# Kernel tuning notes

Hardware: AMD Instinct MI355X
Metric: run time of the kernel (lower is better)

Reference implementation:

```python
import jax, jax.numpy as jnp
import numpy as np

EPS = 1e-7
C_IN = 1.0
C_ATTN = 1.0
C_OUT = 1.0
B, N, D_IN, H, D_OUT = 4, 2048, 128, 8, 64  # in_features = D_IN+1, ambient A = D_OUT+1
INIT_BOUND = 0.02


def _lift(spatial, c):
    # lift spatial coords to hyperboloid of curvature c: x0 = sqrt(1/c + ||x_s||^2)
    time = jnp.sqrt(1.0 / c + jnp.sum(spatial * spatial, axis=-1, keepdims=True))
    return jnp.concatenate([time, spatial], axis=-1)


def _lorentz_normalize(mu, c):
    # project weighted sum back onto hyperboloid: mu / (sqrt(c) * sqrt(|<mu,mu>_L|))
    lor = -mu[..., 0:1] ** 2 + jnp.sum(mu[..., 1:] ** 2, axis=-1, keepdims=True)
    return mu / (jnp.sqrt(c) * jnp.sqrt(jnp.clip(-lor, EPS)))


def setup_inputs() -> dict:
    key = jax.random.key(0)
    ks = jax.random.split(key, 8)
    x_spatial = jax.random.normal(ks[0], (B, N, D_IN), dtype=jnp.float32) * 0.5
    x = _lift(x_spatial, C_IN)  # valid hyperboloid points, curvature C_IN
    u = lambda k, shp: jax.random.uniform(k, shp, minval=-INIT_BOUND, maxval=INIT_BOUND, dtype=jnp.float32)
    return {
        "x": x,
        "Wq": u(ks[1], (H, D_IN + 1, D_OUT)),
        "Wk": u(ks[2], (H, D_IN + 1, D_OUT)),
        "Wv": u(ks[3], (H, D_IN + 1, D_OUT)),
        "bq": u(ks[4], (H, D_OUT)),
        "bk": u(ks[5], (H, D_OUT)),
        "bv": u(ks[6], (H, D_OUT)),
        "scale": jnp.array(1.0, dtype=jnp.float32),
        "attn_bias": jnp.array(0.0, dtype=jnp.float32),
    }


def reference(x, Wq, Wk, Wv, bq, bk, bv, scale, attn_bias):
    # HTCLinear per head (vectorized over heads): spatial = x @ W + b, lift to curvature C_ATTN
    def proj(W, b):
        s = jnp.einsum('bni,hid->bnhd', x, W) + b  # (B,N,H,D_OUT)
        return _lift(s, C_ATTN)                    # (B,N,H,D_OUT+1)

    q = proj(Wq, bq)
    k = proj(Wk, bk)
    v = proj(Wv, bv)

    # Lorentzian inner product scores: -q0*k0 + q_s . k_s  -> (B,N,H,M)
    li = (-jnp.einsum('bnh,bmh->bnhm', q[..., 0], k[..., 0])
          + jnp.einsum('bnhd,bmhd->bnhm', q[..., 1:], k[..., 1:]))
    scores = (2.0 + 2.0 * li) / (scale + EPS) + attn_bias
    w = jax.nn.softmax(scores, axis=-1)

    # Lorentz midpoint aggregation over keys
    mu = jnp.einsum('bnhm,bmha->bnha', w, v)
    mid = _lorentz_normalize(mu, C_ATTN)  # (B,N,H,A)

    # uniform Lorentz midpoint over heads (weights 1/H)
    avg = jnp.mean(mid, axis=2)           # (B,N,A)
    out = _lorentz_normalize(avg, C_ATTN)

    # spatial_to_hyperboloid: rescale curvature C_ATTN -> C_OUT and re-lift
    spatial = out[..., 1:] * jnp.sqrt(C_ATTN / C_OUT)
    return _lift(spatial, C_OUT)  # (B,N,D_OUT+1)
```

## Files before the change

kernel.cpp:

```cpp
#include <hip/hip_runtime.h>
#include <hip/hip_bf16.h>

typedef __bf16 bf16x8 __attribute__((ext_vector_type(8)));
typedef float f32x16 __attribute__((ext_vector_type(16)));
typedef unsigned int u32;
typedef unsigned short u16;
typedef u32 u32x2 __attribute__((ext_vector_type(2)));
typedef u32 u32x4 __attribute__((ext_vector_type(4)));

static constexpr int Nn  = 2048;
static constexpr int DIN = 129;
static constexpr int QP  = 80;
static constexpr int AMB = 65;
static constexpr int XP  = 144;
static constexpr int NS  = 2;
static constexpr int PR  = 72;
static constexpr int KROW = 88;
static constexpr int KTS  = 3072;
static constexpr int VROW = 40;
static constexpr int VTS  = 4096;
static constexpr float LOG2E = 1.4426950408889634f;

#define DEV static __device__ __forceinline__

#if __has_builtin(__builtin_amdgcn_exp2f)
#define FEXP2 __builtin_amdgcn_exp2f
#else
#define FEXP2 exp2f
#endif

DEV u16 f2bf(float f) {
  union { __bf16 h; u16 u; } c;
  c.h = (__bf16)f;
  return c.u;
}
DEV float bf2f(u16 u) {
  union { float f; u32 uu; } c;
  c.uu = ((u32)u) << 16;
  return c.f;
}
DEV u32 cvtpk(float a, float b) {
  u32 r;
  asm("v_cvt_pk_bf16_f32 %0, %1, %2" : "=v"(r) : "v"(a), "v"(b));
  return r;
}
DEV void swap32(u32& a, u32& b) {
  asm("v_permlane32_swap_b32 %0, %1" : "+v"(a), "+v"(b));
}
DEV void gload_lds16(const u16* g, u16* l) {
  __builtin_amdgcn_global_load_lds(
      (const __attribute__((address_space(1))) unsigned int*)g,
      (__attribute__((address_space(3))) unsigned int*)l, 16, 0, 0);
}

__global__ __launch_bounds__(256) void prep_k(const float* __restrict__ x,
                                              u16* __restrict__ xb) {
  const int t = blockIdx.x * 256 + threadIdx.x;
  const int row = t / 18, cg = t % 18;
  u16 tmp[8];
#pragma unroll
  for (int j = 0; j < 8; ++j) {
    const int c = cg * 8 + j;
    tmp[j] = (c < DIN) ? f2bf(x[(size_t)row * DIN + c])
                       : (c == DIN ? f2bf(1.0f) : (u16)0);
  }
  u32x4 w;
  w[0] = (u32)tmp[0] | ((u32)tmp[1] << 16);
  w[1] = (u32)tmp[2] | ((u32)tmp[3] << 16);
  w[2] = (u32)tmp[4] | ((u32)tmp[5] << 16);
  w[3] = (u32)tmp[6] | ((u32)tmp[7] << 16);
  *((u32x4*)xb + t) = w;
}

__global__ __launch_bounds__(256) void proj_k(
    const u16* __restrict__ xb,
    const float* __restrict__ Wq, const float* __restrict__ Wk, const float* __restrict__ Wv,
    const float* __restrict__ bq, const float* __restrict__ bk, const float* __restrict__ bv,
    const float* __restrict__ scale_p,
    u16* __restrict__ Qb, u16* __restrict__ Ktl, u16* __restrict__ Vtl) {
  __shared__ u16 wt[64][152];
  __shared__ __align__(16) u16 tiles[4][2816];

  const int tid = threadIdx.x;
  const int wid = tid >> 6, l = tid & 63;
  const int z = blockIdx.y;
  const int T = z >> 3, h = z & 7;
  const float* W    = (T == 0 ? Wq : (T == 1 ? Wk : Wv)) + (size_t)h * DIN * 64;
  const float* bias = (T == 0 ? bq : (T == 1 ? bk : bv)) + h * 64;

  {
    const int d = tid & 63, kk = tid >> 6;
    for (int k = kk; k < XP; k += 4)
      wt[d][k] = (k < DIN) ? f2bf(W[(size_t)k * 64 + d])
                           : (k == DIN ? f2bf(bias[d]) : (u16)0);
  }
  __syncthreads();

  const int lo = l & 31, hi = l >> 5;
  const float alpha = 2.0f * LOG2E / (scale_p[0] + 1e-7f);
  u16* tl = &tiles[wid][0];

#pragma unroll 1
  for (int rt = 0; rt < 2; ++rt) {
    const int row0 = (blockIdx.x * 8 + wid * 2 + rt) * 32;
    const u16* xr = xb + (size_t)(row0 + lo) * XP;

    f32x16 acc0 = {}, acc1 = {};
#pragma unroll
    for (int s = 0; s < 9; ++s) {
      bf16x8 a  = *(const bf16x8*)&xr[16 * s + 8 * hi];
      bf16x8 b0 = *(const bf16x8*)&wt[lo][16 * s + 8 * hi];
      bf16x8 b1 = *(const bf16x8*)&wt[32 + lo][16 * s + 8 * hi];
      acc0 = __builtin_amdgcn_mfma_f32_32x32x16_bf16(b0, a, acc0, 0, 0, 0);
      acc1 = __builtin_amdgcn_mfma_f32_32x32x16_bf16(b1, a, acc1, 0, 0, 0);
    }

    float nrm = 0.f;
#pragma unroll
    for (int r = 0; r < 16; ++r) nrm += acc0[r] * acc0[r] + acc1[r] * acc1[r];
    nrm += __shfl_xor(nrm, 32);
    const float time = sqrtf(1.0f + nrm);

    if (T == 0) {
#pragma unroll
      for (int g = 0; g < 4; ++g) {
        const u32 w0 = cvtpk(alpha * acc0[4 * g],     alpha * acc0[4 * g + 1]);
        const u32 w1 = cvtpk(alpha * acc0[4 * g + 2], alpha * acc0[4 * g + 3]);
        const u32 w2 = cvtpk(alpha * acc1[4 * g],     alpha * acc1[4 * g + 1]);
        const u32 w3 = cvtpk(alpha * acc1[4 * g + 2], alpha * acc1[4 * g + 3]);
        *(u32x2*)&tl[lo * 80 + 8 * g + 4 * hi]      = (u32x2){w0, w1};
        *(u32x2*)&tl[lo * 80 + 32 + 8 * g + 4 * hi] = (u32x2){w2, w3};
      }
      if (hi == 0) *(u32x4*)&tl[lo * 80 + 64] = (u32x4){(u32)f2bf(alpha * time), 0, 0, 0};
      else         *(u32x4*)&tl[lo * 80 + 72] = (u32x4){0, 0, 0, 0};
    } else if (T == 1) {
#pragma unroll
      for (int g = 0; g < 4; ++g) {
        const u32 w0 = cvtpk(acc0[4 * g],     acc0[4 * g + 1]);
        const u32 w1 = cvtpk(acc0[4 * g + 2], acc0[4 * g + 3]);
        const u32 w2 = cvtpk(acc1[4 * g],     acc1[4 * g + 1]);
        const u32 w3 = cvtpk(acc1[4 * g + 2], acc1[4 * g + 3]);
        *(u32x2*)&tl[lo * 88 + 8 * g + 4 * hi]      = (u32x2){w0, w1};
        *(u32x2*)&tl[lo * 88 + 32 + 8 * g + 4 * hi] = (u32x2){w2, w3};
      }
      if (hi == 0) *(u32x4*)&tl[lo * 88 + 64] = (u32x4){(u32)f2bf(-(time - 1.0f)), 0, 0, 0};
      else         *(u32x4*)&tl[lo * 88 + 72] = (u32x4){0, 0, 0, 0};
    } else {
#pragma unroll
      for (int r = 0; r < 16; ++r) {
        const int d = (r & 3) + 8 * (r >> 2) + 4 * hi;
        tl[d * 40 + lo]        = f2bf(acc0[r]);
        tl[(32 + d) * 40 + lo] = f2bf(acc1[r]);
      }
      if (hi == 0) tl[64 * 40 + lo] = f2bf(time);
    }

    const int b = row0 >> 11, n0 = row0 & 2047;
    const int bh = b * 8 + h;
    u16* gdst;
    int nch;
    if (T == 0) { gdst = Qb + ((size_t)bh * Nn + n0) * QP;                nch = 320; }
    else if (T == 1) { gdst = Ktl + (size_t)bh * 64 * KTS + (size_t)(n0 >> 5) * KTS; nch = 352; }
    else { gdst = Vtl + (size_t)bh * 64 * VTS + (size_t)(n0 >> 5) * VTS;  nch = 325; }
    for (int j = l; j < nch; j += 64)
      *(u32x4*)(gdst + j * 8) = *(const u32x4*)(tl + j * 8);
  }
}

DEV void stage_super(const u16* kg, const u16* vg, u16* kl, u16* vl,
                     const int w, const int lane) {
  if (w == 0) {
#pragma unroll
    for (int i = 0; i < 6; ++i) gload_lds16(kg + i * 512 + lane * 8, kl + i * 512);
    gload_lds16(vg + lane * 8, vl);
  } else if (w == 1) {
#pragma unroll
    for (int i = 1; i < 8; ++i) gload_lds16(vg + i * 512 + lane * 8, vl + i * 512);
  } else if (w == 2) {
#pragma unroll
    for (int i = 6; i < 12; ++i) gload_lds16(kg + i * 512 + lane * 8, kl + i * 512);
    gload_lds16(vg + 8 * 512 + lane * 8, vl + 8 * 512);
  } else {
#pragma unroll
    for (int i = 9; i < 16; ++i) gload_lds16(vg + i * 512 + lane * 8, vl + i * 512);
  }
}

DEV void waitbar() {
  asm volatile("s_waitcnt vmcnt(0) lgkmcnt(0)\ns_barrier" ::: "memory");
}

DEV void exp_pack(const f32x16 sc, bf16x8& fA, bf16x8& fB) {
  float p[16];
#pragma unroll
  for (int r = 0; r < 16; ++r) p[r] = FEXP2(sc[r]);
  u32 a0 = cvtpk(p[0], p[1]),  a1 = cvtpk(p[2], p[3]);
  u32 a2 = cvtpk(p[4], p[5]),  a3 = cvtpk(p[6], p[7]);
  u32 c0 = cvtpk(p[8], p[9]),  c1 = cvtpk(p[10], p[11]);
  u32 c2 = cvtpk(p[12], p[13]), c3 = cvtpk(p[14], p[15]);
  swap32(a0, a2);
  swap32(a1, a3);
  swap32(c0, c2);
  swap32(c1, c3);
  union { u32x4 u; bf16x8 b; } ca, cb;
  ca.u = (u32x4){a0, a1, a2, a3};
  cb.u = (u32x4){c0, c1, c2, c3};
  fA = ca.b;
  fB = cb.b;
}

DEV void compute_tile64(const u16* kl, const u16* vl, const int lo, const int hi,
                        const bf16x8 (&qA)[5], const bf16x8 (&qB)[5],
                        f32x16& a0, f32x16& a1, f32x16& a2,
                        f32x16& b0, f32x16& b1, f32x16& b2) {
  f32x16 sA = {}, sB = {};
  __builtin_amdgcn_s_setprio(1);
#pragma unroll
  for (int s = 0; s < 5; ++s) {
    const bf16x8 kf = *(const bf16x8*)&kl[lo * KROW + 16 * s + 8 * hi];
    sA = __builtin_amdgcn_mfma_f32_32x32x16_bf16(kf, qA[s], sA, 0, 0, 0);
    sB = __builtin_amdgcn_mfma_f32_32x32x16_bf16(kf, qB[s], sB, 0, 0, 0);
  }
  __builtin_amdgcn_s_setprio(0);
  bf16x8 fA0, fB0, fA1, fB1;
  exp_pack(sA, fA0, fB0);
  exp_pack(sB, fA1, fB1);
  __builtin_amdgcn_s_setprio(1);
#pragma unroll
  for (int t = 0; t < 3; ++t) {
    const bf16x8 va = *(const bf16x8*)&vl[(32 * t + lo) * VROW + 8 * hi];
    const bf16x8 vb = *(const bf16x8*)&vl[(32 * t + lo) * VROW + 16 + 8 * hi];
    f32x16& oa = (t == 0 ? a0 : (t == 1 ? a1 : a2));
    f32x16& ob = (t == 0 ? b0 : (t == 1 ? b1 : b2));
    oa = __builtin_amdgcn_mfma_f32_32x32x16_bf16(va, fA0, oa, 0, 0, 0);
    oa = __builtin_amdgcn_mfma_f32_32x32x16_bf16(vb, fB0, oa, 0, 0, 0);
    ob = __builtin_amdgcn_mfma_f32_32x32x16_bf16(va, fA1, ob, 0, 0, 0);
    ob = __builtin_amdgcn_mfma_f32_32x32x16_bf16(vb, fB1, ob, 0, 0, 0);
  }
  __builtin_amdgcn_s_setprio(0);
}

DEV void write_partial(u16* part, const int bh, const int sidx, const int q,
                       const int hi, const f32x16& o0, const f32x16& o1,
                       const f32x16& o2) {
  u16* po = part + ((size_t)((bh * NS + sidx) * Nn + q)) * PR;
#pragma unroll
  for (int t = 0; t < 4; ++t) {
    const u32 a0 = cvtpk(o0[4 * t], o0[4 * t + 1]);
    const u32 a1 = cvtpk(o0[4 * t + 2], o0[4 * t + 3]);
    const u32 b0 = cvtpk(o1[4 * t], o1[4 * t + 1]);
    const u32 b1 = cvtpk(o1[4 * t + 2], o1[4 * t + 3]);
    *(u32x2*)&po[8 * t + 4 * hi]      = (u32x2){a0, a1};
    *(u32x2*)&po[8 * t + 4 * hi + 32] = (u32x2){b0, b1};
  }
  if (hi == 0) po[64] = f2bf(o2[0]);
}

__global__ __launch_bounds__(256, 2) void attn_k(
    const u16* __restrict__ Qb, const u16* __restrict__ Ktl,
    const u16* __restrict__ Vtl, u16* __restrict__ part) {
  __shared__ u16 kls[2][2 * KTS];
  __shared__ u16 vls[2][2 * VTS];

  const int tid  = threadIdx.x;
  const int w    = tid >> 6, lane = tid & 63;
  const int lo   = lane & 31, hi = lane >> 5;

  const u32 bid = blockIdx.x;
  const u32 swz = (bid & 7) * 64 + (bid >> 3);
  const int bh   = swz >> 4;
  const int sidx = (swz >> 3) & 1;
  const int qt   = swz & 7;
  const int qbase = qt * 256 + w * 64;

  const u16* qrowA = Qb + ((size_t)bh * Nn + qbase + lo) * QP;
  const u16* qrowB = qrowA + 32 * QP;
  bf16x8 qA[5], qB[5];
#pragma unroll
  for (int s = 0; s < 5; ++s) {
    qA[s] = *(const bf16x8*)&qrowA[16 * s + 8 * hi];
    qB[s] = *(const bf16x8*)&qrowB[16 * s + 8 * hi];
  }

  f32x16 a0 = {}, a1 = {}, a2 = {};
  f32x16 b0 = {}, b1 = {}, b2 = {};
  const u16* ktb = Ktl + (size_t)bh * 64 * KTS + (size_t)(sidx * 32) * KTS;
  const u16* vtb = Vtl + (size_t)bh * 64 * VTS + (size_t)(sidx * 32) * VTS;

  stage_super(ktb, vtb, kls[0], vls[0], w, lane);
  waitbar();

#pragma unroll 1
  for (int s = 0; s < 16; ++s) {
    const int pf = (s + 1 < 16) ? s + 1 : 15;
    stage_super(ktb + (size_t)pf * 2 * KTS, vtb + (size_t)pf * 2 * VTS,
                kls[(s + 1) & 1], vls[(s + 1) & 1], w, lane);
    compute_tile64(kls[s & 1],       vls[s & 1],       lo, hi, qA, qB, a0, a1, a2, b0, b1, b2);
    compute_tile64(kls[s & 1] + KTS, vls[s & 1] + VTS, lo, hi, qA, qB, a0, a1, a2, b0, b1, b2);
    waitbar();
  }

  write_partial(part, bh, sidx, qbase + lo,      hi, a0, a1, a2);
  write_partial(part, bh, sidx, qbase + 32 + lo, hi, b0, b1, b2);
}

__global__ __launch_bounds__(256) void finale_k(const u16* __restrict__ part,
                                                float* __restrict__ out) {
  const int tid = threadIdx.x;
  const int wv = tid >> 6, l = tid & 63;
  const int g = blockIdx.x * 4 + wv;
  const int b = g >> 11, n = g & 2047;
  const int h = l >> 3, c = l & 7;

  const u16* rowp = part + ((size_t)((b * 8 + h) * NS) * Nn + n) * PR;
  float Oh[8];
#pragma unroll
  for (int j = 0; j < 8; ++j) Oh[j] = 0.f;
  float th = 0.f;
#pragma unroll
  for (int s = 0; s < NS; ++s) {
    const u16* rp = rowp + (size_t)s * Nn * PR;
    const u32x4 v = *(const u32x4*)&rp[8 * c];
#pragma unroll
    for (int i = 0; i < 4; ++i) {
      union { u32 u; float f; } a, bb;
      a.u  = v[i] << 16;
      bb.u = v[i] & 0xffff0000u;
      Oh[2 * i]     += a.f;
      Oh[2 * i + 1] += bb.f;
    }
    th += bf2f(rp[64]);
  }

  float sq = 0.f;
#pragma unroll
  for (int j = 0; j < 8; ++j) sq += Oh[j] * Oh[j];
  sq += __shfl_xor(sq, 1);
  sq += __shfl_xor(sq, 2);
  sq += __shfl_xor(sq, 4);
  const float invh = rsqrtf(fmaxf(th * th - sq, 1e-7f));

  float S[8];
#pragma unroll
  for (int j = 0; j < 8; ++j) S[j] = Oh[j] * invh;
  float T = th * invh;
#pragma unroll
  for (int m = 8; m <= 32; m <<= 1) {
#pragma unroll
    for (int j = 0; j < 8; ++j) S[j] += __shfl_xor(S[j], m);
    T += __shfl_xor(T, m);
  }

  float s2 = 0.f;
#pragma unroll
  for (int j = 0; j < 8; ++j) s2 += S[j] * S[j];
  s2 += __shfl_xor(s2, 1);
  s2 += __shfl_xor(s2, 2);
  s2 += __shfl_xor(s2, 4);
  const float inv = rsqrtf(fmaxf(T * T - s2, 1e-7f));
  const float ssp = s2 * inv * inv;

  float* o = out + (size_t)g * AMB;
  if (h == 0) {
#pragma unroll
    for (int j = 0; j < 8; ++j) o[1 + 8 * c + j] = S[j] * inv;
    if (l == 0) o[0] = sqrtf(1.0f + ssp);
  }
}

extern "C" void kernel_launch(void* const* d_in, const int* in_sizes, int n_in,
                              void* d_out, int out_size, void* d_ws, size_t ws_size,
                              hipStream_t stream) {
  (void)in_sizes; (void)n_in; (void)out_size; (void)ws_size;
  const float* x  = (const float*)d_in[0];
  const float* Wq = (const float*)d_in[1];
  const float* Wk = (const float*)d_in[2];
  const float* Wv = (const float*)d_in[3];
  const float* bq = (const float*)d_in[4];
  const float* bk = (const float*)d_in[5];
  const float* bv = (const float*)d_in[6];
  const float* sc = (const float*)d_in[7];

  char* ws = (char*)d_ws;
  u16*  Qb  = (u16*)(ws);
  u16*  Ktl = (u16*)(ws + 10485760);
  u16*  Vtl = (u16*)(ws + 23068672);
  u16*  pb  = (u16*)(ws + 39845888);
  u16*  xb  = (u16*)(ws + 39845888);
  float* out = (float*)d_out;

  hipLaunchKernelGGL(prep_k, dim3(576), dim3(256), 0, stream, x, xb);
  hipLaunchKernelGGL(proj_k, dim3(32, 24), dim3(256), 0, stream,
                     xb, Wq, Wk, Wv, bq, bk, bv, sc, Qb, Ktl, Vtl);
  hipLaunchKernelGGL(attn_k, dim3(512), dim3(256), 0, stream, Qb, Ktl, Vtl, pb);
  hipLaunchKernelGGL(finale_k, dim3(2048), dim3(256), 0, stream, pb, out);
}
```

Measured before the change: 84.36 us.

## Split attention keys into four chunks with single-tile staging and higher occupancy

Raises the key-split factor from 2 to 4, so the attention grid doubles to 1024 blocks. Each block now handles 16 single 64-key tiles instead of 16 double-tile steps. LDS buffers shrink to one tile per stage and launch bounds request 4 blocks per CU. The aim is better CU occupancy and more latency hiding on a 256-CU device. In exchange, partial-output traffic doubles and the finale kernel must merge more partials.

After: 265.3 us. +214.5%, slower.

```diff
diff --git a/kernel.cpp b/kernel.cpp
--- a/kernel.cpp
+++ b/kernel.cpp
@@ -13,7 +13,7 @@
 static constexpr int QP  = 80;
 static constexpr int AMB = 65;
 static constexpr int XP  = 144;
-static constexpr int NS  = 2;
+static constexpr int NS  = 4;
 static constexpr int PR  = 72;
 static constexpr int KROW = 88;
 static constexpr int KTS  = 3072;
@@ -167,22 +167,19 @@
   }
 }
 
-DEV void stage_super(const u16* kg, const u16* vg, u16* kl, u16* vl,
-                     const int w, const int lane) {
-  if (w == 0) {
-#pragma unroll
-    for (int i = 0; i < 6; ++i) gload_lds16(kg + i * 512 + lane * 8, kl + i * 512);
-    gload_lds16(vg + lane * 8, vl);
-  } else if (w == 1) {
-#pragma unroll
-    for (int i = 1; i < 8; ++i) gload_lds16(vg + i * 512 + lane * 8, vl + i * 512);
-  } else if (w == 2) {
-#pragma unroll
-    for (int i = 6; i < 12; ++i) gload_lds16(kg + i * 512 + lane * 8, kl + i * 512);
-    gload_lds16(vg + 8 * 512 + lane * 8, vl + 8 * 512);
+DEV void stage_tile(const u16* kg, const u16* vg, u16* kl, u16* vl,
+                    const int w, const int lane) {
+  if (w < 2) {
+#pragma unroll
+    for (int i = 0; i < 3; ++i)
+      gload_lds16(kg + (w * 3 + i) * 512 + lane * 8, kl + (w * 3 + i) * 512);
+    gload_lds16(vg + w * 512 + lane * 8, vl + w * 512);
   } else {
 #pragma unroll
-    for (int i = 9; i < 16; ++i) gload_lds16(vg + i * 512 + lane * 8, vl + i * 512);
+    for (int i = 0; i < 3; ++i) {
+      const int j = (w - 2) * 3 + 2 + i;
+      gload_lds16(vg + j * 512 + lane * 8, vl + j * 512);
+    }
   }
 }
 
@@ -256,20 +253,20 @@
   if (hi == 0) po[64] = f2bf(o2[0]);
 }
 
-__global__ __launch_bounds__(256, 2) void attn_k(
+__global__ __launch_bounds__(256, 4) void attn_k(
     const u16* __restrict__ Qb, const u16* __restrict__ Ktl,
     const u16* __restrict__ Vtl, u16* __restrict__ part) {
-  __shared__ u16 kls[2][2 * KTS];
-  __shared__ u16 vls[2][2 * VTS];
+  __shared__ u16 kls[2][KTS];
+  __shared__ u16 vls[2][VTS];
 
   const int tid  = threadIdx.x;
   const int w    = tid >> 6, lane = tid & 63;
   const int lo   = lane & 31, hi = lane >> 5;
 
   const u32 bid = blockIdx.x;
-  const u32 swz = (bid & 7) * 64 + (bid >> 3);
-  const int bh   = swz >> 4;
-  const int sidx = (swz >> 3) & 1;
+  const u32 swz = (bid & 7) * 128 + (bid >> 3);
+  const int bh   = swz >> 5;
+  const int sidx = (swz >> 3) & 3;
   const int qt   = swz & 7;
   const int qbase = qt * 256 + w * 64;
 
@@ -284,19 +281,18 @@
 
   f32x16 a0 = {}, a1 = {}, a2 = {};
   f32x16 b0 = {}, b1 = {}, b2 = {};
-  const u16* ktb = Ktl + (size_t)bh * 64 * KTS + (size_t)(sidx * 32) * KTS;
-  const u16* vtb = Vtl + (size_t)bh * 64 * VTS + (size_t)(sidx * 32) * VTS;
-
-  stage_super(ktb, vtb, kls[0], vls[0], w, lane);
+  const u16* ktb = Ktl + (size_t)bh * 64 * KTS + (size_t)(sidx * 16) * KTS;
+  const u16* vtb = Vtl + (size_t)bh * 64 * VTS + (size_t)(sidx * 16) * VTS;
+
+  stage_tile(ktb, vtb, kls[0], vls[0], w, lane);
   waitbar();
 
 #pragma unroll 1
-  for (int s = 0; s < 16; ++s) {
-    const int pf = (s + 1 < 16) ? s + 1 : 15;
-    stage_super(ktb + (size_t)pf * 2 * KTS, vtb + (size_t)pf * 2 * VTS,
-                kls[(s + 1) & 1], vls[(s + 1) & 1], w, lane);
-    compute_tile64(kls[s & 1],       vls[s & 1],       lo, hi, qA, qB, a0, a1, a2, b0, b1, b2);
-    compute_tile64(kls[s & 1] + KTS, vls[s & 1] + VTS, lo, hi, qA, qB, a0, a1, a2, b0, b1, b2);
+  for (int t = 0; t < 16; ++t) {
+    const int pf = (t + 1 < 16) ? t + 1 : 15;
+    stage_tile(ktb + (size_t)pf * KTS, vtb + (size_t)pf * VTS,
+               kls[(t + 1) & 1], vls[(t + 1) & 1], w, lane);
+    compute_tile64(kls[t & 1], vls[t & 1], lo, hi, qA, qB, a0, a1, a2, b0, b1, b2);
     waitbar();
   }
 
@@ -392,6 +388,6 @@
   hipLaunchKernelGGL(prep_k, dim3(576), dim3(256), 0, stream, x, xb);
   hipLaunchKernelGGL(proj_k, dim3(32, 24), dim3(256), 0, stream,
                      xb, Wq, Wk, Wv, bq, bk, bv, sc, Qb, Ktl, Vtl);
-  hipLaunchKernelGGL(attn_k, dim3(512), dim3(256), 0, stream, Qb, Ktl, Vtl, pb);
+  hipLaunchKernelGGL(attn_k, dim3(1024), dim3(256), 0, stream, Qb, Ktl, Vtl, pb);
   hipLaunchKernelGGL(finale_k, dim3(2048), dim3(256), 0, stream, pb, out);
 }
```

## Compute time-coordinate row with VALU dot instead of a third MFMA tile

Applied to the files above, without the earlier changes.

The third PV MFMA tile, which existed only to produce the single time-coordinate row of V, is removed. That row is now accumulated with scalar FMAs from the fp32 exp values, followed by a cross-half shuffle reduction. V staging shrinks to 6 chunks per tile and is redistributed evenly across the four waves, reducing LDS footprint and global traffic. This saves a third of the PV MFMAs but adds VALU work and LDS reads in the softmax section.

New measurement: 84.57 us. About the same (+0.2%).

```diff
diff --git a/kernel.cpp b/kernel.cpp
--- a/kernel.cpp
+++ b/kernel.cpp
@@ -19,6 +19,7 @@
 static constexpr int KTS  = 3072;
 static constexpr int VROW = 40;
 static constexpr int VTS  = 4096;
+static constexpr int VLT  = 3072;
 static constexpr float LOG2E = 1.4426950408889634f;
 
 #define DEV static __device__ __forceinline__
@@ -37,6 +38,16 @@
 DEV float bf2f(u16 u) {
   union { float f; u32 uu; } c;
   c.uu = ((u32)u) << 16;
+  return c.f;
+}
+DEV float lo16f(u32 u) {
+  union { float f; u32 uu; } c;
+  c.uu = u << 16;
+  return c.f;
+}
+DEV float hi16f(u32 u) {
+  union { float f; u32 uu; } c;
+  c.uu = u & 0xffff0000u;
   return c.f;
 }
 DEV u32 cvtpk(float a, float b) {
@@ -172,17 +183,15 @@
   if (w == 0) {
 #pragma unroll
     for (int i = 0; i < 6; ++i) gload_lds16(kg + i * 512 + lane * 8, kl + i * 512);
-    gload_lds16(vg + lane * 8, vl);
   } else if (w == 1) {
 #pragma unroll
-    for (int i = 1; i < 8; ++i) gload_lds16(vg + i * 512 + lane * 8, vl + i * 512);
+    for (int i = 0; i < 6; ++i) gload_lds16(kg + KTS + i * 512 + lane * 8, kl + KTS + i * 512);
   } else if (w == 2) {
 #pragma unroll
-    for (int i = 6; i < 12; ++i) gload_lds16(kg + i * 512 + lane * 8, kl + i * 512);
-    gload_lds16(vg + 8 * 512 + lane * 8, vl + 8 * 512);
+    for (int i = 0; i < 6; ++i) gload_lds16(vg + i * 512 + lane * 8, vl + i * 512);
   } else {
 #pragma unroll
-    for (int i = 9; i < 16; ++i) gload_lds16(vg + i * 512 + lane * 8, vl + i * 512);
+    for (int i = 0; i < 6; ++i) gload_lds16(vg + VTS + i * 512 + lane * 8, vl + VLT + i * 512);
   }
 }
 
@@ -190,29 +199,10 @@
   asm volatile("s_waitcnt vmcnt(0) lgkmcnt(0)\ns_barrier" ::: "memory");
 }
 
-DEV void exp_pack(const f32x16 sc, bf16x8& fA, bf16x8& fB) {
-  float p[16];
-#pragma unroll
-  for (int r = 0; r < 16; ++r) p[r] = FEXP2(sc[r]);
-  u32 a0 = cvtpk(p[0], p[1]),  a1 = cvtpk(p[2], p[3]);
-  u32 a2 = cvtpk(p[4], p[5]),  a3 = cvtpk(p[6], p[7]);
-  u32 c0 = cvtpk(p[8], p[9]),  c1 = cvtpk(p[10], p[11]);
-  u32 c2 = cvtpk(p[12], p[13]), c3 = cvtpk(p[14], p[15]);
-  swap32(a0, a2);
-  swap32(a1, a3);
-  swap32(c0, c2);
-  swap32(c1, c3);
-  union { u32x4 u; bf16x8 b; } ca, cb;
-  ca.u = (u32x4){a0, a1, a2, a3};
-  cb.u = (u32x4){c0, c1, c2, c3};
-  fA = ca.b;
-  fB = cb.b;
-}
-
 DEV void compute_tile64(const u16* kl, const u16* vl, const int lo, const int hi,
                         const bf16x8 (&qA)[5], const bf16x8 (&qB)[5],
-                        f32x16& a0, f32x16& a1, f32x16& a2,
-                        f32x16& b0, f32x16& b1, f32x16& b2) {
+                        f32x16& a0, f32x16& a1, f32x16& b0, f32x16& b1,
+                        float& ta, float& tb) {
   f32x16 sA = {}, sB = {};
   __builtin_amdgcn_s_setprio(1);
 #pragma unroll
@@ -222,16 +212,48 @@
     sB = __builtin_amdgcn_mfma_f32_32x32x16_bf16(kf, qB[s], sB, 0, 0, 0);
   }
   __builtin_amdgcn_s_setprio(0);
-  bf16x8 fA0, fB0, fA1, fB1;
-  exp_pack(sA, fA0, fB0);
-  exp_pack(sB, fA1, fB1);
+
+  float pa[16], pb[16];
+#pragma unroll
+  for (int r = 0; r < 16; ++r) pa[r] = FEXP2(sA[r]);
+#pragma unroll
+  for (int r = 0; r < 16; ++r) pb[r] = FEXP2(sB[r]);
+
+  const u16* v0p = vl + 2560 + 4 * hi;
+#pragma unroll
+  for (int g = 0; g < 4; ++g) {
+    const u32x2 vv = *(const u32x2*)&v0p[8 * g];
+    const float v0 = lo16f(vv[0]), v1 = hi16f(vv[0]);
+    const float v2 = lo16f(vv[1]), v3 = hi16f(vv[1]);
+    ta += pa[4 * g] * v0 + pa[4 * g + 1] * v1 + pa[4 * g + 2] * v2 + pa[4 * g + 3] * v3;
+    tb += pb[4 * g] * v0 + pb[4 * g + 1] * v1 + pb[4 * g + 2] * v2 + pb[4 * g + 3] * v3;
+  }
+
+  u32 x0 = cvtpk(pa[0], pa[1]),   x1 = cvtpk(pa[2], pa[3]);
+  u32 x2 = cvtpk(pa[4], pa[5]),   x3 = cvtpk(pa[6], pa[7]);
+  u32 y0 = cvtpk(pa[8], pa[9]),   y1 = cvtpk(pa[10], pa[11]);
+  u32 y2 = cvtpk(pa[12], pa[13]), y3 = cvtpk(pa[14], pa[15]);
+  swap32(x0, x2); swap32(x1, x3); swap32(y0, y2); swap32(y1, y3);
+  union { u32x4 u; bf16x8 b; } cA0, cB0, cA1, cB1;
+  cA0.u = (u32x4){x0, x1, x2, x3};
+  cB0.u = (u32x4){y0, y1, y2, y3};
+  u32 z0 = cvtpk(pb[0], pb[1]),   z1 = cvtpk(pb[2], pb[3]);
+  u32 z2 = cvtpk(pb[4], pb[5]),   z3 = cvtpk(pb[6], pb[7]);
+  u32 t0 = cvtpk(pb[8], pb[9]),   t1 = cvtpk(pb[10], pb[11]);
+  u32 t2 = cvtpk(pb[12], pb[13]), t3 = cvtpk(pb[14], pb[15]);
+  swap32(z0, z2); swap32(z1, z3); swap32(t0, t2); swap32(t1, t3);
+  cA1.u = (u32x4){z0, z1, z2, z3};
+  cB1.u = (u32x4){t0, t1, t2, t3};
+  const bf16x8 fA0 = cA0.b, fB0 = cB0.b;
+  const bf16x8 fA1 = cA1.b, fB1 = cB1.b;
+
   __builtin_amdgcn_s_setprio(1);
 #pragma unroll
-  for (int t = 0; t < 3; ++t) {
+  for (int t = 0; t < 2; ++t) {
     const bf16x8 va = *(const bf16x8*)&vl[(32 * t + lo) * VROW + 8 * hi];
     const bf16x8 vb = *(const bf16x8*)&vl[(32 * t + lo) * VROW + 16 + 8 * hi];
-    f32x16& oa = (t == 0 ? a0 : (t == 1 ? a1 : a2));
-    f32x16& ob = (t == 0 ? b0 : (t == 1 ? b1 : b2));
+    f32x16& oa = (t == 0 ? a0 : a1);
+    f32x16& ob = (t == 0 ? b0 : b1);
     oa = __builtin_amdgcn_mfma_f32_32x32x16_bf16(va, fA0, oa, 0, 0, 0);
     oa = __builtin_amdgcn_mfma_f32_32x32x16_bf16(vb, fB0, oa, 0, 0, 0);
     ob = __builtin_amdgcn_mfma_f32_32x32x16_bf16(va, fA1, ob, 0, 0, 0);
@@ -242,7 +264,7 @@
 
 DEV void write_partial(u16* part, const int bh, const int sidx, const int q,
                        const int hi, const f32x16& o0, const f32x16& o1,
-                       const f32x16& o2) {
+                       const float time) {
   u16* po = part + ((size_t)((bh * NS + sidx) * Nn + q)) * PR;
 #pragma unroll
   for (int t = 0; t < 4; ++t) {
@@ -253,14 +275,14 @@
     *(u32x2*)&po[8 * t + 4 * hi]      = (u32x2){a0, a1};
     *(u32x2*)&po[8 * t + 4 * hi + 32] = (u32x2){b0, b1};
   }
-  if (hi == 0) po[64] = f2bf(o2[0]);
+  if (hi == 0) po[64] = f2bf(time);
 }
 
 __global__ __launch_bounds__(256, 2) void attn_k(
     const u16* __restrict__ Qb, const u16* __restrict__ Ktl,
     const u16* __restrict__ Vtl, u16* __restrict__ part) {
   __shared__ u16 kls[2][2 * KTS];
-  __shared__ u16 vls[2][2 * VTS];
+  __shared__ u16 vls[2][2 * VLT];
 
   const int tid  = threadIdx.x;
   const int w    = tid >> 6, lane = tid & 63;
@@ -282,8 +304,9 @@
     qB[s] = *(const bf16x8*)&qrowB[16 * s + 8 * hi];
   }
 
-  f32x16 a0 = {}, a1 = {}, a2 = {};
-  f32x16 b0 = {}, b1 = {}, b2 = {};
+  f32x16 a0 = {}, a1 = {};
+  f32x16 b0 = {}, b1 = {};
+  float ta = 0.f, tb = 0.f;
   const u16* ktb = Ktl + (size_t)bh * 64 * KTS + (size_t)(sidx * 32) * KTS;
   const u16* vtb = Vtl + (size_t)bh * 64 * VTS + (size_t)(sidx * 32) * VTS;
 
@@ -295,13 +318,16 @@
     const int pf = (s + 1 < 16) ? s + 1 : 15;
     stage_super(ktb + (size_t)pf * 2 * KTS, vtb + (size_t)pf * 2 * VTS,
                 kls[(s + 1) & 1], vls[(s + 1) & 1], w, lane);
-    compute_tile64(kls[s & 1],       vls[s & 1],       lo, hi, qA, qB, a0, a1, a2, b0, b1, b2);
-    compute_tile64(kls[s & 1] + KTS, vls[s & 1] + VTS, lo, hi, qA, qB, a0, a1, a2, b0, b1, b2);
+    compute_tile64(kls[s & 1],       vls[s & 1],       lo, hi, qA, qB, a0, a1, b0, b1, ta, tb);
+    compute_tile64(kls[s & 1] + KTS, vls[s & 1] + VLT, lo, hi, qA, qB, a0, a1, b0, b1, ta, tb);
     waitbar();
   }
 
-  write_partial(part, bh, sidx, qbase + lo,      hi, a0, a1, a2);
-  write_partial(part, bh, sidx, qbase + 32 + lo, hi, b0, b1, b2);
+  ta += __shfl_xor(ta, 32);
+  tb += __shfl_xor(tb, 32);
+
+  write_partial(part, bh, sidx, qbase + lo,      hi, a0, a1, ta);
+  write_partial(part, bh, sidx, qbase + 32 + lo, hi, b0, b1, tb);
 }
 
 __global__ __launch_bounds__(256) void finale_k(const u16* __restrict__ part,
```
